# Optimization experiments

Hardware: AMD Instinct MI355X
Metric: run time of the kernel (lower is better)

The kernel has to match this reference:

```python
import jax, jax.numpy as jnp
import numpy as np

B, C, H, W = 32, 256, 32, 32
HEADS, DH = 8, 32          # MHA9: num_heads=8, dim_head=32, total_dim=256
TOT = HEADS * DH


def setup_inputs() -> dict:
    key = jax.random.key(0)
    ks = jax.random.split(key, 10)
    s = 0.02
    return {
        "x": jax.random.normal(ks[0], (B, C, H, W), dtype=jnp.float32),
        "Wq": jax.random.normal(ks[1], (TOT, C), dtype=jnp.float32) * s,
        "bq": jnp.zeros((TOT,), dtype=jnp.float32),
        "Wk": jax.random.normal(ks[2], (TOT, C), dtype=jnp.float32) * s,
        "bk": jnp.zeros((TOT,), dtype=jnp.float32),
        "Wv": jax.random.normal(ks[3], (TOT, C), dtype=jnp.float32) * s,
        "bv": jnp.zeros((TOT,), dtype=jnp.float32),
        "Wo": jax.random.normal(ks[4], (C, TOT), dtype=jnp.float32) * s,
        "bo": jnp.zeros((C,), dtype=jnp.float32),
        "gamma": jnp.zeros((1,), dtype=jnp.float32),
    }


def reference(x, Wq, bq, Wk, bk, Wv, bv, Wo, bo, gamma):
    b, c, h, w = x.shape
    S = h * w

    def proj(Wt, bt):
        # 1x1 conv == channel matmul; reshape to (B, heads, S, dh)
        y = jnp.einsum('oc,bchw->bohw', Wt, x) + bt[None, :, None, None]
        return y.reshape(b, HEADS, DH, S).transpose(0, 1, 3, 2)

    q = proj(Wq, bq)
    k = proj(Wk, bk)
    v = proj(Wv, bv)

    scale = 1.0 / jnp.sqrt(jnp.asarray(DH, dtype=x.dtype))
    scores = jnp.einsum('bhsd,bhtd->bhst', q, k) * scale  # [B,h,S,S] full matrix
    weights = jax.nn.softmax(scores, axis=-1)
    o = jnp.einsum('bhst,bhtd->bhsd', weights, v)          # [B,h,S,dh]
    o = o.transpose(0, 1, 3, 2).reshape(b, TOT, h, w)
    o = jnp.einsum('oc,bchw->bohw', Wo, o) + bo[None, :, None, None]
    x_ = gamma * o + x   # inner residual of MultiHeadAttention
    return x + x_        # outer residual of MulAttontion
```

## Files before the change

### kernel.cpp

```cpp
#include <hip/hip_runtime.h>
#include <stdint.h>

typedef unsigned short u16;
typedef unsigned int   u32;
typedef __attribute__((ext_vector_type(8))) short bf16x8;
typedef __attribute__((ext_vector_type(4))) short bf16x4;
typedef __attribute__((ext_vector_type(4))) float f32x4;

#define NT ((size_t)8388608)

__device__ __forceinline__ float bf2f(u16 u) {
  union { float f; u32 i; } v; v.i = ((u32)u) << 16; return v.f;
}
__device__ __forceinline__ u16 f2bf(float f) {
  union { float f; u32 i; } v; v.f = f;
  u32 r = (v.i + 0x7fffu + ((v.i >> 16) & 1u)) >> 16;
  return (u16)r;
}
__device__ __forceinline__ u32 fbits(float f) {
  union { float f; u32 i; } v; v.f = f; return v.i;
}
__device__ __forceinline__ int detect_bf16(const u32* __restrict__ xd) {
  u32 w = xd[threadIdx.x & 63];
  u32 e = (w >> 8) & 0x7fu;
  unsigned long long m = __ballot((e >= 0x38u) && (e <= 0x41u));
  return __popcll(m) > 32;
}
__device__ __forceinline__ void gld16(const void* g, void* l) {
  __builtin_amdgcn_global_load_lds((const __attribute__((address_space(1))) u32*)g,
                                   (__attribute__((address_space(3))) u32*)l, 16, 0, 0);
}

__global__ void __launch_bounds__(256) prologue_kernel(const void* __restrict__ xin,
                                                       u16* __restrict__ xT,
                                                       const void* __restrict__ W0, const void* __restrict__ W1,
                                                       const void* __restrict__ W2, const void* __restrict__ b0,
                                                       const void* __restrict__ b1, const void* __restrict__ b2,
                                                       u16* __restrict__ wdst, float* __restrict__ bdst,
                                                       const void* __restrict__ Wo, const void* __restrict__ bo,
                                                       const void* __restrict__ gm, u16* __restrict__ wodst,
                                                       float* __restrict__ bodst) {
  const int blk = blockIdx.x;
  const int tid = threadIdx.x;
  const int isbf = detect_bf16((const u32*)xin);
  if (blk < 2048) {
    const int s0 = (blk & 15) * 64, c0 = ((blk >> 4) & 3) * 64, b = blk >> 6;
    __shared__ u16 T[64][72];
    if (isbf) {
      const u16* xp = (const u16*)xin;
      for (int t = tid; t < 512; t += 256) {
        int r = t >> 3, off = (t & 7) * 8;
        *(uint4*)&T[r][off] = *(const uint4*)(xp + ((size_t)(b * 256 + c0 + r)) * 1024 + s0 + off);
      }
    } else {
      const float* xp = (const float*)xin;
      for (int t = tid; t < 512; t += 256) {
        int r = t >> 3, off = (t & 7) * 8;
        const float* s = xp + ((size_t)(b * 256 + c0 + r)) * 1024 + s0 + off;
#pragma unroll
        for (int u = 0; u < 8; u++) T[r][off + u] = f2bf(s[u]);
      }
    }
    __syncthreads();
    for (int t = tid; t < 512; t += 256) {
      int r = t >> 3, off = (t & 7) * 8;
      union { u16 h[8]; uint4 v; } pk;
#pragma unroll
      for (int u = 0; u < 8; u++) pk.h[u] = T[off + u][r];
      *(uint4*)(xT + ((size_t)(b * 1024 + s0 + r)) * 256 + c0 + off) = pk.v;
    }
  } else if (blk < 2240) {
    const int g = blk - 2048;
    const int which = g >> 6, bk = g & 63;
    const void* Ws = which == 0 ? W0 : which == 1 ? W1 : W2;
    const void* bs = which == 0 ? b0 : which == 1 ? b1 : b2;
    const int idx = bk * 1024 + tid * 4;
    u16* dst = wdst + which * 65536 + idx;
    if (isbf) {
      *(ushort4*)dst = *(const ushort4*)((const u16*)Ws + idx);
    } else {
      const float* s = (const float*)Ws + idx;
      ushort4 o; o.x = f2bf(s[0]); o.y = f2bf(s[1]); o.z = f2bf(s[2]); o.w = f2bf(s[3]);
      *(ushort4*)dst = o;
    }
    if (bk == 0) {
      bdst[which * 256 + tid] = isbf ? bf2f(((const u16*)bs)[tid]) : ((const float*)bs)[tid];
    }
  } else {
    const int g = blk - 2240;
    const int idx = g * 1024 + tid * 4;
    if (isbf) {
      *(ushort4*)(wodst + idx) = *(const ushort4*)((const u16*)Wo + idx);
    } else {
      const float* s = (const float*)Wo + idx;
      ushort4 o; o.x = f2bf(s[0]); o.y = f2bf(s[1]); o.z = f2bf(s[2]); o.w = f2bf(s[3]);
      *(ushort4*)(wodst + idx) = o;
    }
    if (g == 0) {
      bodst[tid] = isbf ? bf2f(((const u16*)bo)[tid]) : ((const float*)bo)[tid];
      if (tid == 0) bodst[256] = isbf ? bf2f(((const u16*)gm)[0]) : ((const float*)gm)[0];
    }
  }
}

__global__ void __launch_bounds__(256) prep_o(const void* __restrict__ Wo, const void* __restrict__ bo,
                                              const void* __restrict__ gm, u16* __restrict__ wdst,
                                              float* __restrict__ bdst, const u32* __restrict__ xdet) {
  const int isbf = detect_bf16(xdet);
  const int idx = blockIdx.x * 1024 + threadIdx.x * 4;
  if (isbf) {
    *(ushort4*)(wdst + idx) = *(const ushort4*)((const u16*)Wo + idx);
  } else {
    const float* s = (const float*)Wo + idx;
    ushort4 o; o.x = f2bf(s[0]); o.y = f2bf(s[1]); o.z = f2bf(s[2]); o.w = f2bf(s[3]);
    *(ushort4*)(wdst + idx) = o;
  }
  if (blockIdx.x == 0) {
    int t = threadIdx.x;
    bdst[t] = isbf ? bf2f(((const u16*)bo)[t]) : ((const float*)bo)[t];
    if (t == 0) bdst[256] = isbf ? bf2f(((const u16*)gm)[0]) : ((const float*)gm)[0];
  }
}

__global__ void __launch_bounds__(256) qkv_gemm(const u16* __restrict__ xT,
                                                const u16* __restrict__ Wall,
                                                const float* __restrict__ ball,
                                                u16* __restrict__ Qb, u16* __restrict__ Kb,
                                                u16* __restrict__ Vb) {
  const int z = blockIdx.z, b = z / 3, which = z - b * 3;
  const int tid = threadIdx.x, lane = tid & 63, wave = tid >> 6;
  const int quad = lane >> 4, l16 = lane & 15;
  const int wm = wave >> 1, wn = wave & 1;
  const u16* xb = xT + (size_t)b * 262144;
  const u16* W = Wall + which * 65536;
  int m0, n0; const u16 *Abase, *Bbase;
  if (which < 2) { m0 = blockIdx.y * 128; n0 = blockIdx.x * 128; Abase = xb; Bbase = W; }
  else           { m0 = blockIdx.x * 128; n0 = blockIdx.y * 128; Abase = W; Bbase = xb; }

  __shared__ u16 Ash[8192], Bsh[8192];
  f32x4 acc[4][4];
#pragma unroll
  for (int i = 0; i < 4; i++)
#pragma unroll
    for (int j = 0; j < 4; j++) acc[i][j] = (f32x4){0.f, 0.f, 0.f, 0.f};

  const int srow = lane >> 3, scol = (lane & 7) * 8;
  for (int k0 = 0; k0 < 256; k0 += 64) {
    __syncthreads();
#pragma unroll
    for (int p = 0; p < 4; p++) {
      const int row = p * 32 + wave * 8;
      gld16(Abase + (size_t)(m0 + row + srow) * 256 + k0 + scol, &Ash[row * 64 + lane * 8]);
      gld16(Bbase + (size_t)(n0 + row + srow) * 256 + k0 + scol, &Bsh[row * 64 + lane * 8]);
    }
    __syncthreads();
#pragma unroll
    for (int kk = 0; kk < 2; kk++) {
      bf16x8 av[4], bv[4];
#pragma unroll
      for (int i = 0; i < 4; i++) av[i] = *(const bf16x8*)&Ash[(wm * 64 + i * 16 + l16) * 64 + kk * 32 + quad * 8];
#pragma unroll
      for (int j = 0; j < 4; j++) bv[j] = *(const bf16x8*)&Bsh[(wn * 64 + j * 16 + l16) * 64 + kk * 32 + quad * 8];
#pragma unroll
      for (int i = 0; i < 4; i++)
#pragma unroll
        for (int j = 0; j < 4; j++)
          acc[i][j] = __builtin_amdgcn_mfma_f32_16x16x32_bf16(av[i], bv[j], acc[i][j], 0, 0, 0);
    }
  }

  const float* bias = ball + which * 256;
  const float scale = (which == 0) ? 0.25503486f : 1.0f;
#pragma unroll
  for (int i = 0; i < 4; i++) {
#pragma unroll
    for (int j = 0; j < 4; j++) {
      const int mb = m0 + wm * 64 + i * 16 + quad * 4;
      const int n = n0 + wn * 64 + j * 16 + l16;
#pragma unroll
      for (int r = 0; r < 4; r++) {
        const int m = mb + r;
        float v = acc[i][j][r];
        if (which < 2) {
          v = (v + bias[n]) * scale;
          u16* D = (which ? Kb : Qb) + (size_t)b * 262144;
          D[(size_t)m * 256 + n] = f2bf(v);
        } else {
          v = v + bias[m];
          (Vb + (size_t)b * 262144)[(size_t)m * 1024 + n] = f2bf(v);
        }
      }
    }
  }
}

__global__ void __launch_bounds__(512) attn_kernel(const u16* __restrict__ Q,
                                                   const u16* __restrict__ K,
                                                   const u16* __restrict__ V,
                                                   u16* __restrict__ O) {
  const int blk = blockIdx.x;
  const int qc = blk >> 8, bh = blk & 255;
  const int b = bh >> 3, h = bh & 7;
  const int tid = threadIdx.x, wave = tid >> 6, lane = tid & 63;
  const int quad = lane >> 4, l16 = lane & 15;
  __shared__ u16 Ksh[128 * 32];
  __shared__ u16 Vsh[32 * 136];
  const u16* Qg = Q + (size_t)b * 262144 + h * 32;
  const u16* Kg = K + (size_t)b * 262144 + h * 32;
  const u16* Vg = V + (size_t)b * 262144 + (size_t)h * 32768;
  const int qw = qc * 256 + wave * 32;

  bf16x8 qf[2];
#pragma unroll
  for (int qt = 0; qt < 2; qt++)
    qf[qt] = *(const bf16x8*)(Qg + (size_t)(qw + qt * 16 + l16) * 256 + quad * 8);

  f32x4 oacc[2][2];
#pragma unroll
  for (int dt = 0; dt < 2; dt++)
#pragma unroll
    for (int qt = 0; qt < 2; qt++) oacc[dt][qt] = (f32x4){0.f, 0.f, 0.f, 0.f};
  float lsum[2] = {0.f, 0.f};

  const int krow = lane >> 2, kcol = (lane & 3) * 8;
  for (int kt0 = 0; kt0 < 1024; kt0 += 128) {
    __syncthreads();
    {
      const int rb = wave * 16;
      gld16(Kg + (size_t)(kt0 + rb + krow) * 256 + kcol, &Ksh[rb * 32 + lane * 8]);
    }
    for (int c = tid; c < 1024; c += 512) {
      const int r = c >> 5, off = (c & 31) * 8;
      if (r < 32) *(uint4*)&Vsh[r * 136 + off] = *(const uint4*)(Vg + (size_t)r * 1024 + kt0 + off);
    }
    __syncthreads();
#pragma unroll
    for (int sub = 0; sub < 4; sub++) {
      const int sk0 = sub * 32;
      bf16x4 pf[2][2];
#pragma unroll
      for (int mt = 0; mt < 2; mt++) {
        const bf16x8 kf = *(const bf16x8*)&Ksh[(sk0 + mt * 16 + l16) * 32 + quad * 8];
        f32x4 sf[2];
#pragma unroll
        for (int qt = 0; qt < 2; qt++)
          sf[qt] = __builtin_amdgcn_mfma_f32_16x16x32_bf16(
              kf, qf[qt], (f32x4){0.f, 0.f, 0.f, 0.f}, 0, 0, 0);
#pragma unroll
        for (int qt = 0; qt < 2; qt++) {
          const float p0 = __builtin_amdgcn_exp2f(sf[qt][0]);
          const float p1 = __builtin_amdgcn_exp2f(sf[qt][1]);
          const float p2 = __builtin_amdgcn_exp2f(sf[qt][2]);
          const float p3 = __builtin_amdgcn_exp2f(sf[qt][3]);
          lsum[qt] += (p0 + p1) + (p2 + p3);
          union { u32 u[2]; bf16x4 v; } pv;
          pv.u[0] = __builtin_amdgcn_perm(fbits(p1), fbits(p0), 0x07060302u);
          pv.u[1] = __builtin_amdgcn_perm(fbits(p3), fbits(p2), 0x07060302u);
          pf[mt][qt] = pv.v;
        }
      }
      bf16x4 vf[2][2];
#pragma unroll
      for (int dt = 0; dt < 2; dt++)
#pragma unroll
        for (int mt = 0; mt < 2; mt++)
          vf[dt][mt] = *(const bf16x4*)&Vsh[(dt * 16 + l16) * 136 + sk0 + mt * 16 + quad * 4];
#pragma unroll
      for (int mt = 0; mt < 2; mt++)
#pragma unroll
        for (int dt = 0; dt < 2; dt++)
#pragma unroll
          for (int qt = 0; qt < 2; qt++)
            oacc[dt][qt] = __builtin_amdgcn_mfma_f32_16x16x16bf16_1k(
                vf[dt][mt], pf[mt][qt], oacc[dt][qt], 0, 0, 0);
    }
  }

  float linv[2];
#pragma unroll
  for (int qt = 0; qt < 2; qt++) {
    float l = lsum[qt];
    l += __shfl_xor(l, 16);
    l += __shfl_xor(l, 32);
    linv[qt] = 1.0f / l;
  }
#pragma unroll
  for (int dt = 0; dt < 2; dt++)
#pragma unroll
    for (int qt = 0; qt < 2; qt++) {
      ushort4 st;
      st.x = f2bf(oacc[dt][qt][0] * linv[qt]);
      st.y = f2bf(oacc[dt][qt][1] * linv[qt]);
      st.z = f2bf(oacc[dt][qt][2] * linv[qt]);
      st.w = f2bf(oacc[dt][qt][3] * linv[qt]);
      *(ushort4*)(O + (size_t)(b * 1024 + qw + qt * 16 + l16) * 256 + h * 32 + dt * 16 + quad * 4) = st;
    }
}

__global__ void __launch_bounds__(256) out_gemm(const u16* __restrict__ WoB,
                                                const float* __restrict__ bg,
                                                const u16* __restrict__ Ob,
                                                const void* __restrict__ xin,
                                                void* __restrict__ outp,
                                                const u32* __restrict__ xdet) {
  const int b = blockIdx.z;
  const int m0 = blockIdx.y * 128, n0 = blockIdx.x * 128;
  const int tid = threadIdx.x, lane = tid & 63, wave = tid >> 6;
  const int quad = lane >> 4, l16 = lane & 15;
  const int wm = wave >> 1, wn = wave & 1;
  const int isbf = detect_bf16(xdet);
  const u16* Bb = Ob + (size_t)b * 262144;
  __shared__ u16 Ash[8192], Bsh[8192];
  f32x4 acc[4][4];
#pragma unroll
  for (int i = 0; i < 4; i++)
#pragma unroll
    for (int j = 0; j < 4; j++) acc[i][j] = (f32x4){0.f, 0.f, 0.f, 0.f};

  const int srow = lane >> 3, scol = (lane & 7) * 8;
  for (int k0 = 0; k0 < 256; k0 += 64) {
    __syncthreads();
#pragma unroll
    for (int p = 0; p < 4; p++) {
      const int row = p * 32 + wave * 8;
      gld16(WoB + (size_t)(m0 + row + srow) * 256 + k0 + scol, &Ash[row * 64 + lane * 8]);
      gld16(Bb  + (size_t)(n0 + row + srow) * 256 + k0 + scol, &Bsh[row * 64 + lane * 8]);
    }
    __syncthreads();
#pragma unroll
    for (int kk = 0; kk < 2; kk++) {
      bf16x8 av[4], bv[4];
#pragma unroll
      for (int i = 0; i < 4; i++) av[i] = *(const bf16x8*)&Ash[(wm * 64 + i * 16 + l16) * 64 + kk * 32 + quad * 8];
#pragma unroll
      for (int j = 0; j < 4; j++) bv[j] = *(const bf16x8*)&Bsh[(wn * 64 + j * 16 + l16) * 64 + kk * 32 + quad * 8];
#pragma unroll
      for (int i = 0; i < 4; i++)
#pragma unroll
        for (int j = 0; j < 4; j++)
          acc[i][j] = __builtin_amdgcn_mfma_f32_16x16x32_bf16(av[i], bv[j], acc[i][j], 0, 0, 0);
    }
  }

  const float g = bg[256];
#pragma unroll
  for (int i = 0; i < 4; i++) {
#pragma unroll
    for (int j = 0; j < 4; j++) {
      const int mb = m0 + wm * 64 + i * 16 + quad * 4;
      const int n = n0 + wn * 64 + j * 16 + l16;
#pragma unroll
      for (int r = 0; r < 4; r++) {
        const int m = mb + r;
        const float v = acc[i][j][r] + bg[m];
        const size_t gi = (size_t)b * 262144 + (size_t)m * 1024 + n;
        const float xv = isbf ? bf2f(((const u16*)xin)[gi]) : ((const float*)xin)[gi];
        const float res = 2.f * xv + g * v;
        if (isbf) ((u16*)outp)[gi] = f2bf(res);
        else      ((float*)outp)[gi] = res;
      }
    }
  }
}

extern "C" void kernel_launch(void* const* d_in, const int* in_sizes, int n_in,
                              void* d_out, int out_size, void* d_ws, size_t ws_size,
                              hipStream_t stream) {
  const void* x  = d_in[0];
  const void* Wq = d_in[1]; const void* bq = d_in[2];
  const void* Wk = d_in[3]; const void* bk = d_in[4];
  const void* Wv = d_in[5]; const void* bv = d_in[6];
  const void* Wo = d_in[7]; const void* bo = d_in[8];
  const void* gm = d_in[9];

  u16* ws = (u16*)d_ws;
  u16* xT = ws;
  u16* Qb = ws + NT;
  u16* Kb = ws + 2 * NT;
  u16* Vb = ws + 3 * NT;
  u16* Ob = xT;
  const u32* xdet = (const u32*)x;

  u16* WqkvB = (u16*)d_out;
  float* bqkvF = (float*)((u16*)d_out + 196608);

  const bool tail = ws_size >= (size_t)(4 * NT + 66048) * 2;
  u16* WoB = tail ? (ws + 4 * NT) : Qb;
  float* boF = tail ? (float*)(ws + 4 * NT + 65536) : (float*)(Qb + 65536);

  prologue_kernel<<<dim3(tail ? 2304 : 2240), 256, 0, stream>>>(
      x, xT, Wq, Wk, Wv, bq, bk, bv, WqkvB, bqkvF, Wo, bo, gm, WoB, boF);
  qkv_gemm<<<dim3(2, 8, 96), 256, 0, stream>>>(xT, WqkvB, bqkvF, Qb, Kb, Vb);
  attn_kernel<<<dim3(1024), 512, 0, stream>>>(Qb, Kb, Vb, Ob);
  if (!tail) prep_o<<<dim3(64), 256, 0, stream>>>(Wo, bo, gm, WoB, boF, xdet);
  out_gemm<<<dim3(8, 2, 32), 256, 0, stream>>>(WoB, boF, Ob, x, d_out, xdet);
}
```

Measured before the change: 221.6 us.

## Rewrite attention inner loop with 32x32 MFMA, double-buffered swizzled LDS

The attention kernel moves from 16x16 MFMA tiles to 32x32x16 bf16 MFMAs for both QK^T and PV, and builds the P operand in registers with packed bf16 conversion and permlane32 swaps. K and V tiles are double-buffered in XOR-swizzled LDS using async global-to-LDS loads, so the next tile's load overlaps compute and one barrier per tile is dropped. It also adds s_setprio around the MFMAs and an occupancy hint in the launch bounds. The aim is higher matrix-core throughput with fewer LDS bank conflicts and less load stall, at the cost of more complex indexing and higher LDS use.

After: 210.5 us. -5.0%, faster.

```diff
diff --git a/kernel.cpp b/kernel.cpp
--- a/kernel.cpp
+++ b/kernel.cpp
@@ -6,6 +6,7 @@
 typedef __attribute__((ext_vector_type(8))) short bf16x8;
 typedef __attribute__((ext_vector_type(4))) short bf16x4;
 typedef __attribute__((ext_vector_type(4))) float f32x4;
+typedef __attribute__((ext_vector_type(16))) float f32x16;
 
 #define NT ((size_t)8388608)
 
@@ -194,17 +195,17 @@
   }
 }
 
-__global__ void __launch_bounds__(512) attn_kernel(const u16* __restrict__ Q,
-                                                   const u16* __restrict__ K,
-                                                   const u16* __restrict__ V,
-                                                   u16* __restrict__ O) {
+__global__ void __launch_bounds__(512, 4) attn_kernel(const u16* __restrict__ Q,
+                                                      const u16* __restrict__ K,
+                                                      const u16* __restrict__ V,
+                                                      u16* __restrict__ O) {
   const int blk = blockIdx.x;
   const int qc = blk >> 8, bh = blk & 255;
   const int b = bh >> 3, h = bh & 7;
   const int tid = threadIdx.x, wave = tid >> 6, lane = tid & 63;
-  const int quad = lane >> 4, l16 = lane & 15;
-  __shared__ u16 Ksh[128 * 32];
-  __shared__ u16 Vsh[32 * 136];
+  const int hi = lane >> 5, l32 = lane & 31;
+  __shared__ __align__(16) u16 Ksh[2][128 * 32];
+  __shared__ __align__(16) u16 Vsh[2][32 * 128];
   const u16* Qg = Q + (size_t)b * 262144 + h * 32;
   const u16* Kg = K + (size_t)b * 262144 + h * 32;
   const u16* Vg = V + (size_t)b * 262144 + (size_t)h * 32768;
@@ -212,89 +213,135 @@
 
   bf16x8 qf[2];
 #pragma unroll
-  for (int qt = 0; qt < 2; qt++)
-    qf[qt] = *(const bf16x8*)(Qg + (size_t)(qw + qt * 16 + l16) * 256 + quad * 8);
-
-  f32x4 oacc[2][2];
-#pragma unroll
-  for (int dt = 0; dt < 2; dt++)
-#pragma unroll
-    for (int qt = 0; qt < 2; qt++) oacc[dt][qt] = (f32x4){0.f, 0.f, 0.f, 0.f};
-  float lsum[2] = {0.f, 0.f};
-
-  const int krow = lane >> 2, kcol = (lane & 3) * 8;
-  for (int kt0 = 0; kt0 < 1024; kt0 += 128) {
-    __syncthreads();
-    {
-      const int rb = wave * 16;
-      gld16(Kg + (size_t)(kt0 + rb + krow) * 256 + kcol, &Ksh[rb * 32 + lane * 8]);
-    }
-    for (int c = tid; c < 1024; c += 512) {
-      const int r = c >> 5, off = (c & 31) * 8;
-      if (r < 32) *(uint4*)&Vsh[r * 136 + off] = *(const uint4*)(Vg + (size_t)r * 1024 + kt0 + off);
-    }
-    __syncthreads();
-#pragma unroll
-    for (int sub = 0; sub < 4; sub++) {
-      const int sk0 = sub * 32;
-      bf16x4 pf[2][2];
-#pragma unroll
-      for (int mt = 0; mt < 2; mt++) {
-        const bf16x8 kf = *(const bf16x8*)&Ksh[(sk0 + mt * 16 + l16) * 32 + quad * 8];
-        f32x4 sf[2];
-#pragma unroll
-        for (int qt = 0; qt < 2; qt++)
-          sf[qt] = __builtin_amdgcn_mfma_f32_16x16x32_bf16(
-              kf, qf[qt], (f32x4){0.f, 0.f, 0.f, 0.f}, 0, 0, 0);
-#pragma unroll
-        for (int qt = 0; qt < 2; qt++) {
-          const float p0 = __builtin_amdgcn_exp2f(sf[qt][0]);
-          const float p1 = __builtin_amdgcn_exp2f(sf[qt][1]);
-          const float p2 = __builtin_amdgcn_exp2f(sf[qt][2]);
-          const float p3 = __builtin_amdgcn_exp2f(sf[qt][3]);
-          lsum[qt] += (p0 + p1) + (p2 + p3);
-          union { u32 u[2]; bf16x4 v; } pv;
-          pv.u[0] = __builtin_amdgcn_perm(fbits(p1), fbits(p0), 0x07060302u);
-          pv.u[1] = __builtin_amdgcn_perm(fbits(p3), fbits(p2), 0x07060302u);
-          pf[mt][qt] = pv.v;
-        }
-      }
-      bf16x4 vf[2][2];
-#pragma unroll
-      for (int dt = 0; dt < 2; dt++)
-#pragma unroll
-        for (int mt = 0; mt < 2; mt++)
-          vf[dt][mt] = *(const bf16x4*)&Vsh[(dt * 16 + l16) * 136 + sk0 + mt * 16 + quad * 4];
-#pragma unroll
-      for (int mt = 0; mt < 2; mt++)
-#pragma unroll
-        for (int dt = 0; dt < 2; dt++)
-#pragma unroll
-          for (int qt = 0; qt < 2; qt++)
-            oacc[dt][qt] = __builtin_amdgcn_mfma_f32_16x16x16bf16_1k(
-                vf[dt][mt], pf[mt][qt], oacc[dt][qt], 0, 0, 0);
-    }
-  }
-
-  float linv[2];
-#pragma unroll
-  for (int qt = 0; qt < 2; qt++) {
-    float l = lsum[qt];
-    l += __shfl_xor(l, 16);
-    l += __shfl_xor(l, 32);
-    linv[qt] = 1.0f / l;
-  }
-#pragma unroll
-  for (int dt = 0; dt < 2; dt++)
-#pragma unroll
-    for (int qt = 0; qt < 2; qt++) {
-      ushort4 st;
-      st.x = f2bf(oacc[dt][qt][0] * linv[qt]);
-      st.y = f2bf(oacc[dt][qt][1] * linv[qt]);
-      st.z = f2bf(oacc[dt][qt][2] * linv[qt]);
-      st.w = f2bf(oacc[dt][qt][3] * linv[qt]);
-      *(ushort4*)(O + (size_t)(b * 1024 + qw + qt * 16 + l16) * 256 + h * 32 + dt * 16 + quad * 4) = st;
-    }
+  for (int ks = 0; ks < 2; ks++)
+    qf[ks] = *(const bf16x8*)(Qg + (size_t)(qw + l32) * 256 + ks * 16 + hi * 8);
+
+  const int Gg = wave * 64 + lane;
+  const int th = Gg >> 3;
+  const int uu = (Gg & 7) ^ (th & 7);
+  const u16* ksrc = Kg + (size_t)(th * 2 + (uu >> 2)) * 256 + (uu & 3) * 8;
+  u16* kdst0 = &Ksh[0][Gg * 8];
+  u16* kdst1 = &Ksh[1][Gg * 8];
+  const int vd = tid >> 4;
+  const u16* vsrc = Vg + (size_t)vd * 1024 + ((tid & 15) ^ (vd & 15)) * 8;
+  u16* vdst0 = &Vsh[0][tid * 8];
+  u16* vdst1 = &Vsh[1][tid * 8];
+
+  const int kkey = (l32 >> 1) & 7;
+  const int kb0 = (l32 >> 1) * 128 + (((((l32 & 1) << 2) | 0 | hi) ^ kkey) << 4);
+  const int kb1 = (l32 >> 1) * 128 + (((((l32 & 1) << 2) | 2 | hi) ^ kkey) << 4);
+  int vb[4];
+#pragma unroll
+  for (int tt = 0; tt < 4; tt++) vb[tt] = l32 * 256 + (((l32 & 12) ^ (tt << 2)) << 4);
+  const int vm0 = ((l32 & 3) ^ hi) << 4;
+  const int vm1 = ((l32 & 3) ^ (2 | hi)) << 4;
+
+  f32x16 oacc;
+#pragma unroll
+  for (int r = 0; r < 16; r++) oacc[r] = 0.f;
+  float lsum = 0.f;
+
+  gld16(ksrc, kdst0);
+  gld16(vsrc, vdst0);
+  __syncthreads();
+
+#pragma unroll 1
+  for (int kt = 0; kt < 8; kt++) {
+    const int c = kt & 1;
+    if (kt < 7) {
+      gld16(ksrc + (size_t)(kt + 1) * 32768, c ? kdst0 : kdst1);
+      gld16(vsrc + (kt + 1) * 128,           c ? vdst0 : vdst1);
+    }
+    const char* Kb = (const char*)&Ksh[c][0];
+    const char* Vb = (const char*)&Vsh[c][0];
+#pragma unroll
+    for (int tt = 0; tt < 4; tt++) {
+      const bf16x8 kf0 = *(const bf16x8*)(Kb + tt * 2048 + kb0);
+      const bf16x8 kf1 = *(const bf16x8*)(Kb + tt * 2048 + kb1);
+      const bf16x8 vf0 = *(const bf16x8*)(Vb + vb[tt] + vm0);
+      const bf16x8 vf1 = *(const bf16x8*)(Vb + vb[tt] + vm1);
+      f32x16 sf;
+#pragma unroll
+      for (int r = 0; r < 16; r++) sf[r] = 0.f;
+      __builtin_amdgcn_s_setprio(1);
+      sf = __builtin_amdgcn_mfma_f32_32x32x16_bf16(kf0, qf[0], sf, 0, 0, 0);
+      sf = __builtin_amdgcn_mfma_f32_32x32x16_bf16(kf1, qf[1], sf, 0, 0, 0);
+      __builtin_amdgcn_s_setprio(0);
+      {
+        const float p0 = __builtin_amdgcn_exp2f(sf[0]);
+        const float p1 = __builtin_amdgcn_exp2f(sf[1]);
+        const float p2 = __builtin_amdgcn_exp2f(sf[2]);
+        const float p3 = __builtin_amdgcn_exp2f(sf[3]);
+        const float p4 = __builtin_amdgcn_exp2f(sf[4]);
+        const float p5 = __builtin_amdgcn_exp2f(sf[5]);
+        const float p6 = __builtin_amdgcn_exp2f(sf[6]);
+        const float p7 = __builtin_amdgcn_exp2f(sf[7]);
+        lsum += ((p0 + p1) + (p2 + p3)) + ((p4 + p5) + (p6 + p7));
+        u32 wa, wb, wc, wd;
+        asm("v_cvt_pk_bf16_f32 %0, %1, %2" : "=v"(wa) : "v"(p0), "v"(p1));
+        asm("v_cvt_pk_bf16_f32 %0, %1, %2" : "=v"(wb) : "v"(p2), "v"(p3));
+        asm("v_cvt_pk_bf16_f32 %0, %1, %2" : "=v"(wc) : "v"(p4), "v"(p5));
+        asm("v_cvt_pk_bf16_f32 %0, %1, %2" : "=v"(wd) : "v"(p6), "v"(p7));
+#if __has_builtin(__builtin_amdgcn_permlane32_swap)
+        auto s0 = __builtin_amdgcn_permlane32_swap((int)wc, (int)wa, false, false);
+        auto s1 = __builtin_amdgcn_permlane32_swap((int)wd, (int)wb, false, false);
+        union { int w[4]; bf16x8 v; } pk;
+        pk.w[0] = s0[1]; pk.w[1] = s1[1]; pk.w[2] = s0[0]; pk.w[3] = s1[0];
+#else
+        const u32 xa = __shfl_xor((int)wa, 32), xb = __shfl_xor((int)wb, 32);
+        const u32 xc = __shfl_xor((int)wc, 32), xd = __shfl_xor((int)wd, 32);
+        union { u32 w[4]; bf16x8 v; } pk;
+        pk.w[0] = hi ? xc : wa; pk.w[1] = hi ? xd : wb;
+        pk.w[2] = hi ? wc : xa; pk.w[3] = hi ? wd : xb;
+#endif
+        __builtin_amdgcn_s_setprio(1);
+        oacc = __builtin_amdgcn_mfma_f32_32x32x16_bf16(pk.v, vf0, oacc, 0, 0, 0);
+        __builtin_amdgcn_s_setprio(0);
+      }
+      {
+        const float p0 = __builtin_amdgcn_exp2f(sf[8]);
+        const float p1 = __builtin_amdgcn_exp2f(sf[9]);
+        const float p2 = __builtin_amdgcn_exp2f(sf[10]);
+        const float p3 = __builtin_amdgcn_exp2f(sf[11]);
+        const float p4 = __builtin_amdgcn_exp2f(sf[12]);
+        const float p5 = __builtin_amdgcn_exp2f(sf[13]);
+        const float p6 = __builtin_amdgcn_exp2f(sf[14]);
+        const float p7 = __builtin_amdgcn_exp2f(sf[15]);
+        lsum += ((p0 + p1) + (p2 + p3)) + ((p4 + p5) + (p6 + p7));
+        u32 wa, wb, wc, wd;
+        asm("v_cvt_pk_bf16_f32 %0, %1, %2" : "=v"(wa) : "v"(p0), "v"(p1));
+        asm("v_cvt_pk_bf16_f32 %0, %1, %2" : "=v"(wb) : "v"(p2), "v"(p3));
+        asm("v_cvt_pk_bf16_f32 %0, %1, %2" : "=v"(wc) : "v"(p4), "v"(p5));
+        asm("v_cvt_pk_bf16_f32 %0, %1, %2" : "=v"(wd) : "v"(p6), "v"(p7));
+#if __has_builtin(__builtin_amdgcn_permlane32_swap)
+        auto s0 = __builtin_amdgcn_permlane32_swap((int)wc, (int)wa, false, false);
+        auto s1 = __builtin_amdgcn_permlane32_swap((int)wd, (int)wb, false, false);
+        union { int w[4]; bf16x8 v; } pk;
+        pk.w[0] = s0[1]; pk.w[1] = s1[1]; pk.w[2] = s0[0]; pk.w[3] = s1[0];
+#else
+        const u32 xa = __shfl_xor((int)wa, 32), xb = __shfl_xor((int)wb, 32);
+        const u32 xc = __shfl_xor((int)wc, 32), xd = __shfl_xor((int)wd, 32);
+        union { u32 w[4]; bf16x8 v; } pk;
+        pk.w[0] = hi ? xc : wa; pk.w[1] = hi ? xd : wb;
+        pk.w[2] = hi ? wc : xa; pk.w[3] = hi ? wd : xb;
+#endif
+        __builtin_amdgcn_s_setprio(1);
+        oacc = __builtin_amdgcn_mfma_f32_32x32x16_bf16(pk.v, vf1, oacc, 0, 0, 0);
+        __builtin_amdgcn_s_setprio(0);
+      }
+    }
+    if (kt < 7) __syncthreads();
+  }
+
+  lsum += __shfl_xor(lsum, 32);
+  const float linv = 1.0f / lsum;
+  u16* Og = O + (size_t)(b * 1024 + qw) * 256 + h * 32 + l32;
+#pragma unroll
+  for (int r = 0; r < 16; r++) {
+    const int qo = (r & 3) + 8 * (r >> 2) + 4 * hi;
+    const float li = __shfl(linv, qo);
+    Og[(size_t)qo * 256] = f2bf(oacc[r] * li);
+  }
 }
 
 __global__ void __launch_bounds__(256) out_gemm(const u16* __restrict__ WoB,
```
